# Kernel tuning notes

Measured on AMD Instinct MI355X. Metric: run time of the kernel, lower is better.

Reference implementation:

```python
import jax, jax.numpy as jnp
import numpy as np

I, H, O = 3, 50, 1

def setup_inputs() -> dict:
    key = jax.random.key(0)
    ks = jax.random.split(key, 7)
    B, T = 4096, 512
    s_ih = 1.0 / np.sqrt(H)
    x = jax.random.normal(ks[0], (B, T, I), dtype=jnp.float32)
    W_ih = jax.random.uniform(ks[1], (3 * H, I), jnp.float32, -s_ih, s_ih)
    W_hh = jax.random.uniform(ks[2], (3 * H, H), jnp.float32, -s_ih, s_ih)
    b_ih = jax.random.uniform(ks[3], (3 * H,), jnp.float32, -s_ih, s_ih)
    b_hh = jax.random.uniform(ks[4], (3 * H,), jnp.float32, -s_ih, s_ih)
    W_fc = jax.random.uniform(ks[5], (O, H), jnp.float32, -s_ih, s_ih)
    b_fc = jax.random.uniform(ks[6], (O,), jnp.float32, -s_ih, s_ih)
    return {"x": x, "W_ih": W_ih, "W_hh": W_hh, "b_ih": b_ih, "b_hh": b_hh,
            "W_fc": W_fc, "b_fc": b_fc}

def _gru_last_hidden(x, W_ih, W_hh, b_ih, b_hh):
    # x: [B, T, I]. Precompute input projections for all timesteps (one big GEMM).
    B, T, _ = x.shape
    gi = jnp.einsum('bti,gi->btg', x, W_ih) + b_ih  # [B, T, 3H]
    gi = jnp.moveaxis(gi, 1, 0)  # [T, B, 3H] for scan over time

    W_hr, W_hz, W_hn = W_hh[:H], W_hh[H:2*H], W_hh[2*H:]
    b_hr, b_hz, b_hn = b_hh[:H], b_hh[H:2*H], b_hh[2*H:]

    def step(h, gi_t):
        gir, giz, gin = gi_t[:, :H], gi_t[:, H:2*H], gi_t[:, 2*H:]
        r = jax.nn.sigmoid(gir + h @ W_hr.T + b_hr)
        z = jax.nn.sigmoid(giz + h @ W_hz.T + b_hz)
        n = jnp.tanh(gin + r * (h @ W_hn.T + b_hn))
        h_new = (1.0 - z) * n + z * h
        return h_new, None

    h0 = jnp.zeros((B, H), dtype=x.dtype)
    h_last, _ = jax.lax.scan(step, h0, gi)
    return h_last  # [B, H]

def reference(x, W_ih, W_hh, b_ih, b_hh, W_fc, b_fc):
    h_last = _gru_last_hidden(x, W_ih, W_hh, b_ih, b_hh)
    out = h_last @ W_fc.T + b_fc  # [B, 1]
    return out.squeeze(-1)  # [B]
```

## Files before the change

### kernel.cpp

```cpp
#include <hip/hip_runtime.h>
#include <hip/hip_bf16.h>

#define T_LEN 512
#define HID 50
#define NBATCH 4096

using short8  = __attribute__((ext_vector_type(8))) short;
using floatx4 = __attribute__((ext_vector_type(4))) float;

__device__ __forceinline__ float sigm(float v) {
  return __builtin_amdgcn_rcpf(1.0f + __builtin_amdgcn_exp2f(-1.442695041f * v));
}
__device__ __forceinline__ float tanh_f(float v) {
  return 1.0f - 2.0f * __builtin_amdgcn_rcpf(1.0f + __builtin_amdgcn_exp2f(2.885390082f * v));
}
__device__ __forceinline__ unsigned short bf16hi(float v) {
  __hip_bfloat16 b = __float2bfloat16(v);
  return *(unsigned short*)&b;
}
__device__ __forceinline__ float bf16tof(unsigned short u) {
  return __uint_as_float((unsigned int)u << 16);
}

__global__ __launch_bounds__(256, 1)
void gru_mfma_kernel(const float* __restrict__ x,
                     const float* __restrict__ W_ih,
                     const float* __restrict__ W_hh,
                     const float* __restrict__ b_ih,
                     const float* __restrict__ b_hh,
                     const float* __restrict__ W_fc,
                     const float* __restrict__ b_fc,
                     float* __restrict__ out) {
  __shared__ alignas(16) unsigned char lds[16384];
  char* xs   = (char*)lds;
  char* hbuf = (char*)lds + 12288;

  const int tid  = threadIdx.x;
  const int lane = tid & 63;
  const int w    = tid >> 6;
  const int ucol = lane & 15;
  const int kg   = (lane >> 4) & 3;
  const int b0   = blockIdx.x * 16;
  const int u    = 16 * w + ucol;
  const bool uv  = (u < HID);

  const float wfc = uv ? W_fc[u] : 0.f;

  short8 Bh[3][2], Bl[3][2];
  short8 Bch, Bcl;
#pragma unroll
  for (int g = 0; g < 3; ++g) {
#pragma unroll
    for (int f = 0; f < 2; ++f) {
      union { short a[8]; short8 s; } ph, pl;
#pragma unroll
      for (int e = 0; e < 8; ++e) {
        const int k = 32 * f + 8 * kg + e;
        float v = 0.f;
        if (uv) {
          if (k < HID) v = W_hh[(g * 50 + u) * HID + k];
          else if (g < 2) {
            if (k <= 52)      v = W_ih[(g * 50 + u) * 3 + (k - 50)];
            else if (k == 53) v = b_ih[g * 50 + u] + b_hh[g * 50 + u];
            else if (k <= 56) v = W_ih[(g * 50 + u) * 3 + (k - 54)];
          } else {
            if (k == 53)      v = b_hh[100 + u];
          }
        }
        const unsigned short hi = bf16hi(v);
        const unsigned short lo = bf16hi(v - bf16tof(hi));
        ph.a[e] = (short)hi; pl.a[e] = (short)lo;
      }
      Bh[g][f] = ph.s; Bl[g][f] = pl.s;
    }
  }
  {
    union { short a[8]; short8 s; } ph, pl;
#pragma unroll
    for (int e = 0; e < 8; ++e) {
      const int k = 32 + 8 * kg + e;
      float v = 0.f;
      if (uv) {
        if (k >= 50 && k <= 52)      v = W_ih[(100 + u) * 3 + (k - 50)];
        else if (k == 53)            v = b_ih[100 + u];
        else if (k >= 54 && k <= 56) v = W_ih[(100 + u) * 3 + (k - 54)];
      }
      const unsigned short hi = bf16hi(v);
      const unsigned short lo = bf16hi(v - bf16tof(hi));
      ph.a[e] = (short)hi; pl.a[e] = (short)lo;
    }
    Bch = ph.s; Bcl = pl.s;
  }

  ((float4*)hbuf)[tid] = make_float4(0.f, 0.f, 0.f, 0.f);
  __syncthreads();
  if (tid < 64) {
    const int m = tid & 15, c = tid >> 4;
    char* p0 = hbuf + m * 128;
    const int xr = (m & 7) << 4;
    if (c == 3) {
      *(unsigned short*)(p0 + ((2 * 53) ^ xr)) = 0x3F80;
    } else {
      const float xv = x[(size_t)(b0 + m) * (T_LEN * 3) + c];
      const unsigned short hi = bf16hi(xv);
      *(unsigned short*)(p0 + ((2 * (50 + c)) ^ xr)) = hi;
      *(unsigned short*)(p0 + ((2 * (54 + c)) ^ xr)) = bf16hi(xv - bf16tof(hi));
    }
  }

  float h[4] = {0.f, 0.f, 0.f, 0.f};
  const int arow = ucol * 128;
  const int axr  = (ucol & 7) << 4;
  const floatx4 z4 = {0.f, 0.f, 0.f, 0.f};

  int hoff[4];
#pragma unroll
  for (int r = 0; r < 4; ++r) {
    const int m = 4 * kg + r;
    hoff[r] = m * 128 + ((2 * u) ^ ((m & 7) << 4));
  }
  int xc = (ucol >= 6) ? (ucol - 6) : (ucol - 2);
  xc = xc < 0 ? 0 : (xc > 2 ? 2 : xc);
  const int xcol   = (ucol >= 6) ? (54 + xc) : (ucol == 5 ? 53 : 50 + xc);
  const bool isOne = (ucol == 5);
  const bool isHi  = (ucol >= 2 && ucol <= 4);
  const bool isH1  = (ucol < 2);
  int soff[4], xroff[4];
#pragma unroll
  for (int r = 0; r < 4; ++r) {
    const int m = 4 * kg + r;
    soff[r]  = isH1 ? hoff[r] : (m * 128 + ((2 * xcol) ^ ((m & 7) << 4)));
    xroff[r] = xc * 64 + m * 4;
  }

  for (int tc = 0; tc < 8; ++tc) {
    {
      const int sm = tid >> 4, seg = tid & 15;
      const float* xb = x + (size_t)(b0 + sm) * (T_LEN * 3) + tc * 192 + 3 + seg * 12;
      float vv[12];
      if (tc == 7 && seg == 15) {
#pragma unroll
        for (int j = 0; j < 12; ++j) vv[j] = (j < 9) ? xb[j] : 0.f;
      } else {
        const float4 v0 = *(const float4*)(xb + 0);
        const float4 v1 = *(const float4*)(xb + 4);
        const float4 v2 = *(const float4*)(xb + 8);
        vv[0]=v0.x; vv[1]=v0.y; vv[2]=v0.z; vv[3]=v0.w;
        vv[4]=v1.x; vv[5]=v1.y; vv[6]=v1.z; vv[7]=v1.w;
        vv[8]=v2.x; vv[9]=v2.y; vv[10]=v2.z; vv[11]=v2.w;
      }
#pragma unroll
      for (int jj = 0; jj < 12; ++jj) {
        const int i = seg * 12 + jj;
        *(float*)(xs + (i / 3) * 192 + (i % 3) * 64 + sm * 4) = vv[jj];
      }
    }
    __syncthreads();

#pragma unroll 2
    for (int s = 0; s < 64; ++s) {
      const int par = s & 1;
      const char* rp = hbuf + par * 2048;
      char*       wp = hbuf + (par ^ 1) * 2048;

      const short8 A0 = *(const short8*)(rp + arow + ((16 * kg)      ^ axr));
      const short8 A1 = *(const short8*)(rp + arow + ((16 * kg + 64) ^ axr));

      floatx4 r1 = __builtin_amdgcn_mfma_f32_16x16x32_bf16(A0, Bh[0][0], z4, 0, 0, 0);
      r1 = __builtin_amdgcn_mfma_f32_16x16x32_bf16(A1, Bh[0][1], r1, 0, 0, 0);
      floatx4 r2 = __builtin_amdgcn_mfma_f32_16x16x32_bf16(A0, Bl[0][0], z4, 0, 0, 0);
      r2 = __builtin_amdgcn_mfma_f32_16x16x32_bf16(A1, Bl[0][1], r2, 0, 0, 0);
      floatx4 zA = __builtin_amdgcn_mfma_f32_16x16x32_bf16(A0, Bh[1][0], z4, 0, 0, 0);
      zA = __builtin_amdgcn_mfma_f32_16x16x32_bf16(A1, Bh[1][1], zA, 0, 0, 0);
      floatx4 zB = __builtin_amdgcn_mfma_f32_16x16x32_bf16(A0, Bl[1][0], z4, 0, 0, 0);
      zB = __builtin_amdgcn_mfma_f32_16x16x32_bf16(A1, Bl[1][1], zB, 0, 0, 0);
      floatx4 nA = __builtin_amdgcn_mfma_f32_16x16x32_bf16(A0, Bh[2][0], z4, 0, 0, 0);
      nA = __builtin_amdgcn_mfma_f32_16x16x32_bf16(A1, Bh[2][1], nA, 0, 0, 0);
      floatx4 nB = __builtin_amdgcn_mfma_f32_16x16x32_bf16(A0, Bl[2][0], z4, 0, 0, 0);
      nB = __builtin_amdgcn_mfma_f32_16x16x32_bf16(A1, Bl[2][1], nB, 0, 0, 0);
      floatx4 c1 = __builtin_amdgcn_mfma_f32_16x16x32_bf16(A1, Bch, z4, 0, 0, 0);
      floatx4 c2 = __builtin_amdgcn_mfma_f32_16x16x32_bf16(A1, Bcl, c1, 0, 0, 0);

      unsigned short hb[4];
#pragma unroll
      for (int r = 0; r < 4; ++r) {
        const float rr = sigm(r1[r] + r2[r]);
        const float zz = sigm(zA[r] + zB[r]);
        const float nv = fmaf(rr, nA[r] + nB[r], c2[r]);
        const float nn = tanh_f(nv);
        h[r] = fmaf(zz, h[r] - nn, nn);
        hb[r] = bf16hi(h[r]);
      }

      if (w < 3) {
#pragma unroll
        for (int r = 0; r < 4; ++r)
          *(unsigned short*)(wp + hoff[r]) = hb[r];
      } else {
#pragma unroll
        for (int r = 0; r < 4; ++r) {
          const float xv = *(const float*)(xs + s * 192 + xroff[r]);
          const unsigned short hi = bf16hi(xv);
          const unsigned short lo = bf16hi(xv - bf16tof(hi));
          unsigned short val = isHi ? hi : lo;
          val = isOne ? (unsigned short)0x3F80 : val;
          val = isH1 ? hb[r] : val;
          if (ucol <= 8)
            *(unsigned short*)(wp + soff[r]) = val;
        }
      }
      __syncthreads();
    }
  }

  float p[4];
#pragma unroll
  for (int r = 0; r < 4; ++r) p[r] = h[r] * wfc;
#pragma unroll
  for (int mask = 1; mask < 16; mask <<= 1) {
#pragma unroll
    for (int r = 0; r < 4; ++r) p[r] += __shfl_xor(p[r], mask);
  }
  if (ucol == 0) {
    *(float4*)(lds + (w * 16 + 4 * kg) * 4) = make_float4(p[0], p[1], p[2], p[3]);
  }
  __syncthreads();
  if (tid < 16) {
    float ssum = 0.f;
#pragma unroll
    for (int ww = 0; ww < 4; ++ww) ssum += *(const float*)(lds + (ww * 16 + tid) * 4);
    out[b0 + tid] = ssum + b_fc[0];
  }
}

extern "C" void kernel_launch(void* const* d_in, const int* in_sizes, int n_in,
                              void* d_out, int out_size, void* d_ws, size_t ws_size,
                              hipStream_t stream) {
  const float* x    = (const float*)d_in[0];
  const float* W_ih = (const float*)d_in[1];
  const float* W_hh = (const float*)d_in[2];
  const float* b_ih = (const float*)d_in[3];
  const float* b_hh = (const float*)d_in[4];
  const float* W_fc = (const float*)d_in[5];
  const float* b_fc = (const float*)d_in[6];
  float* out = (float*)d_out;

  dim3 grid(NBATCH / 16);
  dim3 block(256);
  gru_mfma_kernel<<<grid, block, 0, stream>>>(x, W_ih, W_hh, b_ih, b_hh, W_fc, b_fc, out);
}
```

Baseline: 266.2 us.

## Split 16-row batch tile into two independent 8-row recurrence chains

Each block's 16 batch rows are split into two 8-row groups with separate double-buffered hidden-state tiles in LDS. Each step runs two independent MFMA chains and two sets of gate math, and only half the lanes write results. The aim is to interleave two independent dependency chains and hide MFMA and transcendental latency in the serial time loop. The cost is twice the MFMA instructions and activation work per step, because each 16-row MFMA tile now carries 8 duplicated rows.

```diff
diff --git a/kernel.cpp b/kernel.cpp
--- a/kernel.cpp
+++ b/kernel.cpp
@@ -95,29 +95,31 @@
   ((float4*)hbuf)[tid] = make_float4(0.f, 0.f, 0.f, 0.f);
   __syncthreads();
   if (tid < 64) {
-    const int m = tid & 15, c = tid >> 4;
-    char* p0 = hbuf + m * 128;
-    const int xr = (m & 7) << 4;
+    const int g = tid >> 5, idx = tid & 31;
+    const int m = idx & 7, c = idx >> 3;
+    char* p0 = hbuf + g * 2048 + m * 128;
+    const int xr = m << 4;
     if (c == 3) {
       *(unsigned short*)(p0 + ((2 * 53) ^ xr)) = 0x3F80;
     } else {
-      const float xv = x[(size_t)(b0 + m) * (T_LEN * 3) + c];
+      const float xv = x[(size_t)(b0 + g * 8 + m) * (T_LEN * 3) + c];
       const unsigned short hi = bf16hi(xv);
       *(unsigned short*)(p0 + ((2 * (50 + c)) ^ xr)) = hi;
       *(unsigned short*)(p0 + ((2 * (54 + c)) ^ xr)) = bf16hi(xv - bf16tof(hi));
     }
   }
 
-  float h[4] = {0.f, 0.f, 0.f, 0.f};
-  const int arow = ucol * 128;
+  float hA[4] = {0.f, 0.f, 0.f, 0.f};
+  float hB[4] = {0.f, 0.f, 0.f, 0.f};
+  const int arow = (ucol & 7) * 128;
   const int axr  = (ucol & 7) << 4;
   const floatx4 z4 = {0.f, 0.f, 0.f, 0.f};
 
   int hoff[4];
 #pragma unroll
   for (int r = 0; r < 4; ++r) {
-    const int m = 4 * kg + r;
-    hoff[r] = m * 128 + ((2 * u) ^ ((m & 7) << 4));
+    const int m = (4 * kg + r) & 7;
+    hoff[r] = m * 128 + ((2 * u) ^ (m << 4));
   }
   int xc = (ucol >= 6) ? (ucol - 6) : (ucol - 2);
   xc = xc < 0 ? 0 : (xc > 2 ? 2 : xc);
@@ -128,8 +130,8 @@
   int soff[4], xroff[4];
 #pragma unroll
   for (int r = 0; r < 4; ++r) {
-    const int m = 4 * kg + r;
-    soff[r]  = isH1 ? hoff[r] : (m * 128 + ((2 * xcol) ^ ((m & 7) << 4)));
+    const int m = (4 * kg + r) & 7;
+    soff[r]  = isH1 ? hoff[r] : (m * 128 + ((2 * xcol) ^ (m << 4)));
     xroff[r] = xc * 64 + m * 4;
   }
 
@@ -160,75 +162,116 @@
 #pragma unroll 2
     for (int s = 0; s < 64; ++s) {
       const int par = s & 1;
-      const char* rp = hbuf + par * 2048;
-      char*       wp = hbuf + (par ^ 1) * 2048;
-
-      const short8 A0 = *(const short8*)(rp + arow + ((16 * kg)      ^ axr));
-      const short8 A1 = *(const short8*)(rp + arow + ((16 * kg + 64) ^ axr));
-
-      floatx4 r1 = __builtin_amdgcn_mfma_f32_16x16x32_bf16(A0, Bh[0][0], z4, 0, 0, 0);
-      r1 = __builtin_amdgcn_mfma_f32_16x16x32_bf16(A1, Bh[0][1], r1, 0, 0, 0);
-      floatx4 r2 = __builtin_amdgcn_mfma_f32_16x16x32_bf16(A0, Bl[0][0], z4, 0, 0, 0);
-      r2 = __builtin_amdgcn_mfma_f32_16x16x32_bf16(A1, Bl[0][1], r2, 0, 0, 0);
-      floatx4 zA = __builtin_amdgcn_mfma_f32_16x16x32_bf16(A0, Bh[1][0], z4, 0, 0, 0);
-      zA = __builtin_amdgcn_mfma_f32_16x16x32_bf16(A1, Bh[1][1], zA, 0, 0, 0);
-      floatx4 zB = __builtin_amdgcn_mfma_f32_16x16x32_bf16(A0, Bl[1][0], z4, 0, 0, 0);
-      zB = __builtin_amdgcn_mfma_f32_16x16x32_bf16(A1, Bl[1][1], zB, 0, 0, 0);
-      floatx4 nA = __builtin_amdgcn_mfma_f32_16x16x32_bf16(A0, Bh[2][0], z4, 0, 0, 0);
-      nA = __builtin_amdgcn_mfma_f32_16x16x32_bf16(A1, Bh[2][1], nA, 0, 0, 0);
-      floatx4 nB = __builtin_amdgcn_mfma_f32_16x16x32_bf16(A0, Bl[2][0], z4, 0, 0, 0);
-      nB = __builtin_amdgcn_mfma_f32_16x16x32_bf16(A1, Bl[2][1], nB, 0, 0, 0);
-      floatx4 c1 = __builtin_amdgcn_mfma_f32_16x16x32_bf16(A1, Bch, z4, 0, 0, 0);
-      floatx4 c2 = __builtin_amdgcn_mfma_f32_16x16x32_bf16(A1, Bcl, c1, 0, 0, 0);
-
-      unsigned short hb[4];
+      const char* rp0 = hbuf + par * 1024;
+      const char* rp1 = hbuf + 2048 + par * 1024;
+      char*       wp0 = hbuf + (par ^ 1) * 1024;
+      char*       wp1 = hbuf + 2048 + (par ^ 1) * 1024;
+
+      const short8 A00 = *(const short8*)(rp0 + arow + ((16 * kg)      ^ axr));
+      const short8 A01 = *(const short8*)(rp0 + arow + ((16 * kg + 64) ^ axr));
+      const short8 A10 = *(const short8*)(rp1 + arow + ((16 * kg)      ^ axr));
+      const short8 A11 = *(const short8*)(rp1 + arow + ((16 * kg + 64) ^ axr));
+
+      floatx4 r1a = __builtin_amdgcn_mfma_f32_16x16x32_bf16(A00, Bh[0][0], z4, 0, 0, 0);
+      r1a = __builtin_amdgcn_mfma_f32_16x16x32_bf16(A01, Bh[0][1], r1a, 0, 0, 0);
+      floatx4 r2a = __builtin_amdgcn_mfma_f32_16x16x32_bf16(A00, Bl[0][0], z4, 0, 0, 0);
+      r2a = __builtin_amdgcn_mfma_f32_16x16x32_bf16(A01, Bl[0][1], r2a, 0, 0, 0);
+      floatx4 zAa = __builtin_amdgcn_mfma_f32_16x16x32_bf16(A00, Bh[1][0], z4, 0, 0, 0);
+      zAa = __builtin_amdgcn_mfma_f32_16x16x32_bf16(A01, Bh[1][1], zAa, 0, 0, 0);
+      floatx4 zBa = __builtin_amdgcn_mfma_f32_16x16x32_bf16(A00, Bl[1][0], z4, 0, 0, 0);
+      zBa = __builtin_amdgcn_mfma_f32_16x16x32_bf16(A01, Bl[1][1], zBa, 0, 0, 0);
+      floatx4 nAa = __builtin_amdgcn_mfma_f32_16x16x32_bf16(A00, Bh[2][0], z4, 0, 0, 0);
+      nAa = __builtin_amdgcn_mfma_f32_16x16x32_bf16(A01, Bh[2][1], nAa, 0, 0, 0);
+      floatx4 nBa = __builtin_amdgcn_mfma_f32_16x16x32_bf16(A00, Bl[2][0], z4, 0, 0, 0);
+      nBa = __builtin_amdgcn_mfma_f32_16x16x32_bf16(A01, Bl[2][1], nBa, 0, 0, 0);
+      floatx4 cCa = __builtin_amdgcn_mfma_f32_16x16x32_bf16(A01, Bch, z4, 0, 0, 0);
+      cCa = __builtin_amdgcn_mfma_f32_16x16x32_bf16(A01, Bcl, cCa, 0, 0, 0);
+
+      floatx4 r1b = __builtin_amdgcn_mfma_f32_16x16x32_bf16(A10, Bh[0][0], z4, 0, 0, 0);
+      r1b = __builtin_amdgcn_mfma_f32_16x16x32_bf16(A11, Bh[0][1], r1b, 0, 0, 0);
+      floatx4 r2b = __builtin_amdgcn_mfma_f32_16x16x32_bf16(A10, Bl[0][0], z4, 0, 0, 0);
+      r2b = __builtin_amdgcn_mfma_f32_16x16x32_bf16(A11, Bl[0][1], r2b, 0, 0, 0);
+      floatx4 zAb = __builtin_amdgcn_mfma_f32_16x16x32_bf16(A10, Bh[1][0], z4, 0, 0, 0);
+      zAb = __builtin_amdgcn_mfma_f32_16x16x32_bf16(A11, Bh[1][1], zAb, 0, 0, 0);
+      floatx4 zBb = __builtin_amdgcn_mfma_f32_16x16x32_bf16(A10, Bl[1][0], z4, 0, 0, 0);
+      zBb = __builtin_amdgcn_mfma_f32_16x16x32_bf16(A11, Bl[1][1], zBb, 0, 0, 0);
+      floatx4 nAb = __builtin_amdgcn_mfma_f32_16x16x32_bf16(A10, Bh[2][0], z4, 0, 0, 0);
+      nAb = __builtin_amdgcn_mfma_f32_16x16x32_bf16(A11, Bh[2][1], nAb, 0, 0, 0);
+      floatx4 nBb = __builtin_amdgcn_mfma_f32_16x16x32_bf16(A10, Bl[2][0], z4, 0, 0, 0);
+      nBb = __builtin_amdgcn_mfma_f32_16x16x32_bf16(A11, Bl[2][1], nBb, 0, 0, 0);
+      floatx4 cCb = __builtin_amdgcn_mfma_f32_16x16x32_bf16(A11, Bch, z4, 0, 0, 0);
+      cCb = __builtin_amdgcn_mfma_f32_16x16x32_bf16(A11, Bcl, cCb, 0, 0, 0);
+
+      unsigned short hbA[4], hbB[4];
 #pragma unroll
       for (int r = 0; r < 4; ++r) {
-        const float rr = sigm(r1[r] + r2[r]);
-        const float zz = sigm(zA[r] + zB[r]);
-        const float nv = fmaf(rr, nA[r] + nB[r], c2[r]);
-        const float nn = tanh_f(nv);
-        h[r] = fmaf(zz, h[r] - nn, nn);
-        hb[r] = bf16hi(h[r]);
+        const float rr = sigm(r1a[r] + r2a[r]);
+        const float zz = sigm(zAa[r] + zBa[r]);
+        const float nn = tanh_f(fmaf(rr, nAa[r] + nBa[r], cCa[r]));
+        hA[r] = fmaf(zz, hA[r] - nn, nn);
+        hbA[r] = bf16hi(hA[r]);
+      }
+#pragma unroll
+      for (int r = 0; r < 4; ++r) {
+        const float rr = sigm(r1b[r] + r2b[r]);
+        const float zz = sigm(zAb[r] + zBb[r]);
+        const float nn = tanh_f(fmaf(rr, nAb[r] + nBb[r], cCb[r]));
+        hB[r] = fmaf(zz, hB[r] - nn, nn);
+        hbB[r] = bf16hi(hB[r]);
       }
 
       if (w < 3) {
-#pragma unroll
-        for (int r = 0; r < 4; ++r)
-          *(unsigned short*)(wp + hoff[r]) = hb[r];
+        if (kg < 2) {
+#pragma unroll
+          for (int r = 0; r < 4; ++r) {
+            *(unsigned short*)(wp0 + hoff[r]) = hbA[r];
+            *(unsigned short*)(wp1 + hoff[r]) = hbB[r];
+          }
+        }
       } else {
-#pragma unroll
-        for (int r = 0; r < 4; ++r) {
-          const float xv = *(const float*)(xs + s * 192 + xroff[r]);
-          const unsigned short hi = bf16hi(xv);
-          const unsigned short lo = bf16hi(xv - bf16tof(hi));
-          unsigned short val = isHi ? hi : lo;
-          val = isOne ? (unsigned short)0x3F80 : val;
-          val = isH1 ? hb[r] : val;
-          if (ucol <= 8)
-            *(unsigned short*)(wp + soff[r]) = val;
+        if (kg < 2 && ucol <= 8) {
+#pragma unroll
+          for (int r = 0; r < 4; ++r) {
+            const float xvA = *(const float*)(xs + s * 192 + xroff[r]);
+            const float xvB = *(const float*)(xs + s * 192 + 32 + xroff[r]);
+            const unsigned short hiA = bf16hi(xvA);
+            const unsigned short hiB = bf16hi(xvB);
+            unsigned short vA = isHi ? hiA : bf16hi(xvA - bf16tof(hiA));
+            unsigned short vB = isHi ? hiB : bf16hi(xvB - bf16tof(hiB));
+            vA = isOne ? (unsigned short)0x3F80 : vA;
+            vB = isOne ? (unsigned short)0x3F80 : vB;
+            vA = isH1 ? hbA[r] : vA;
+            vB = isH1 ? hbB[r] : vB;
+            *(unsigned short*)(wp0 + soff[r]) = vA;
+            *(unsigned short*)(wp1 + soff[r]) = vB;
+          }
         }
       }
       __syncthreads();
     }
   }
 
-  float p[4];
-#pragma unroll
-  for (int r = 0; r < 4; ++r) p[r] = h[r] * wfc;
+  float pA[4], pB[4];
+#pragma unroll
+  for (int r = 0; r < 4; ++r) { pA[r] = hA[r] * wfc; pB[r] = hB[r] * wfc; }
 #pragma unroll
   for (int mask = 1; mask < 16; mask <<= 1) {
 #pragma unroll
-    for (int r = 0; r < 4; ++r) p[r] += __shfl_xor(p[r], mask);
-  }
-  if (ucol == 0) {
-    *(float4*)(lds + (w * 16 + 4 * kg) * 4) = make_float4(p[0], p[1], p[2], p[3]);
+    for (int r = 0; r < 4; ++r) {
+      pA[r] += __shfl_xor(pA[r], mask);
+      pB[r] += __shfl_xor(pB[r], mask);
+    }
+  }
+  if (ucol == 0 && kg < 2) {
+    float* sl = (float*)lds + w * 16;
+    *(float4*)(sl + kg * 4)     = make_float4(pA[0], pA[1], pA[2], pA[3]);
+    *(float4*)(sl + 8 + kg * 4) = make_float4(pB[0], pB[1], pB[2], pB[3]);
   }
   __syncthreads();
   if (tid < 16) {
     float ssum = 0.f;
 #pragma unroll
-    for (int ww = 0; ww < 4; ++ww) ssum += *(const float*)(lds + (ww * 16 + tid) * 4);
+    for (int ww = 0; ww < 4; ++ww) ssum += ((const float*)lds)[ww * 16 + tid];
     out[b0 + tid] = ssum + b_fc[0];
   }
 }
```

After: 457.3 us. 1.72x slower.
